# Kernel tuning notes

Measured on AMD Instinct MI355X. Metric: run time of the kernel, lower is better.

Reference implementation:

```python
import jax, jax.numpy as jnp
import numpy as np

B = 2
D = 256          # d_model == q_model
NH = 8           # heads
DH = D // NH
NP = 4           # sampling points per level
LV = 4           # feature levels
NQ = 4096        # queries
NL = 6           # encoder layers
DFF = 1024
SHAPES = [(128, 128), (64, 64), (32, 32), (16, 16)]
S = sum(h * w for h, w in SHAPES)


def setup_inputs() -> dict:
    key = jax.random.key(0)
    ks = iter(jax.random.split(key, 64))
    d = {}
    for l, (h, w) in enumerate(SHAPES):
        d[f"src{l}"] = jax.random.normal(next(ks), (B, D, h, w), jnp.float32)
        d[f"pos{l}"] = jax.random.normal(next(ks), (B, D, h, w), jnp.float32)
        d[f"mask{l}"] = jnp.zeros((B, h, w), jnp.bool_)
    d["q_feat"] = jax.random.normal(next(ks), (B, NQ, D), jnp.float32)
    d["q_pos"] = jax.random.normal(next(ks), (B, NQ, D), jnp.float32)
    d["q_ref"] = jax.random.uniform(next(ks), (B, NQ, 2), jnp.float32)
    d["level_embed"] = jax.random.normal(next(ks), (LV, D), jnp.float32) * 0.02

    def p(shape):
        return jax.random.normal(next(ks), shape, jnp.float32) * 0.02

    d["so_w"] = p((NL, NH * LV * NP * 2, D)); d["so_b"] = p((NL, NH * LV * NP * 2))
    d["aw_w"] = p((NL, NH * LV * NP, D));     d["aw_b"] = p((NL, NH * LV * NP))
    d["vp_w"] = p((NL, D, D)); d["vp_b"] = p((NL, D))
    d["op_w"] = p((NL, D, D)); d["op_b"] = p((NL, D))
    d["n1_g"] = jnp.ones((NL, D)); d["n1_b"] = jnp.zeros((NL, D))
    d["l1_w"] = p((NL, DFF, D)); d["l1_b"] = p((NL, DFF))
    d["l2_w"] = p((NL, D, DFF)); d["l2_b"] = p((NL, D))
    d["n2_g"] = jnp.ones((NL, D)); d["n2_b"] = jnp.zeros((NL, D))
    return d


def _ln(x, g, b):
    m = x.mean(-1, keepdims=True)
    v = ((x - m) ** 2).mean(-1, keepdims=True)
    return (x - m) * jax.lax.rsqrt(v + 1e-5) * g + b


def _bilinear(v, loc, Hl, Wl):
    # v: [B,NH,Hl*Wl,DH], loc: [B,NH,NQ,NP,2] normalized to [0,1]
    # grid_sample semantics, align_corners=False, zero padding
    x = loc[..., 0] * Wl - 0.5
    y = loc[..., 1] * Hl - 0.5
    x0 = jnp.floor(x); y0 = jnp.floor(y)
    wx = x - x0; wy = y - y0
    out = jnp.zeros((B, NH, NQ, NP, DH), v.dtype)
    for dx, dy in ((0, 0), (1, 0), (0, 1), (1, 1)):
        xc = x0 + dx; yc = y0 + dy
        w = (wx if dx else 1.0 - wx) * (wy if dy else 1.0 - wy)
        valid = (xc >= 0) & (xc < Wl) & (yc >= 0) & (yc < Hl)
        xi = jnp.clip(xc, 0, Wl - 1).astype(jnp.int32)
        yi = jnp.clip(yc, 0, Hl - 1).astype(jnp.int32)
        idx = (yi * Wl + xi).reshape(B, NH, NQ * NP)
        g = jnp.take_along_axis(v, idx[..., None], axis=2).reshape(B, NH, NQ, NP, DH)
        out = out + g * (w * valid)[..., None]
    return out


def _msda(q, ref, value, pad_mask, so_w, so_b, aw_w, aw_b, vp_w, vp_b, op_w, op_b):
    # q: [B,NQ,D]; ref: [B,NQ,LV,2]; value: [B,S,D]; pad_mask: [B,S] bool
    v = jnp.einsum('bsd,ed->bse', value, vp_w) + vp_b
    v = jnp.where(pad_mask[..., None], 0.0, v)
    v = v.reshape(B, S, NH, DH).transpose(0, 2, 1, 3)  # [B,NH,S,DH]
    offs = (jnp.einsum('bqd,od->bqo', q, so_w) + so_b).reshape(B, NQ, NH, LV, NP, 2)
    aw = (jnp.einsum('bqd,od->bqo', q, aw_w) + aw_b).reshape(B, NQ, NH, LV * NP)
    aw = jax.nn.softmax(aw, axis=-1).reshape(B, NQ, NH, LV, NP)
    norm = jnp.array([[w, h] for h, w in SHAPES], jnp.float32)  # (W,H) per level
    loc = ref[:, :, None, :, None, :] + offs / norm[None, None, None, :, None, :]
    loc = loc.transpose(0, 2, 1, 3, 4, 5)  # [B,NH,NQ,LV,NP,2]
    start = 0
    samp = []
    for l, (Hl, Wl) in enumerate(SHAPES):
        vl = v[:, :, start:start + Hl * Wl]
        start += Hl * Wl
        samp.append(_bilinear(vl, loc[:, :, :, l], Hl, Wl))
    samp = jnp.stack(samp, axis=3)  # [B,NH,NQ,LV,NP,DH]
    out = jnp.einsum('bhqlpd,bqhlp->bqhd', samp, aw).reshape(B, NQ, D)
    return jnp.einsum('bqd,od->bqo', out, op_w) + op_b


def _forward(srcs, poss, masks, q_feat, q_pos, q_ref, level_embed,
             so_w, so_b, aw_w, aw_b, vp_w, vp_b, op_w, op_b,
             n1_g, n1_b, l1_w, l1_b, l2_w, l2_b, n2_g, n2_b):
    src_flat, mask_flat = [], []
    for lvl, (s, m, p) in enumerate(zip(srcs, masks, poss)):
        b, c, h, w = s.shape
        src_flat.append(s.reshape(b, c, h * w).transpose(0, 2, 1))
        mask_flat.append(m.reshape(b, h * w))
        # lvl_pos_embed = p + level_embed[lvl]  (computed in torch but unused by layers)
    src_flat = jnp.concatenate(src_flat, axis=1)   # [B,S,D]
    mask_flat = jnp.concatenate(mask_flat, axis=1)  # [B,S]
    vrs = []
    for m in masks:
        _, H, W = m.shape
        vH = jnp.sum(~m[:, :, 0], axis=1).astype(jnp.float32) / H
        vW = jnp.sum(~m[:, 0, :], axis=1).astype(jnp.float32) / W
        vrs.append(jnp.stack([vW, vH], axis=-1))
    valid_ratios = jnp.stack(vrs, axis=1)  # [B,LV,2]
    ref = q_ref[:, :, None, :] * valid_ratios[:, None]  # [B,NQ,LV,2]
    qf = q_feat
    for l in range(NL):
        src2 = _msda(qf + q_pos, ref, src_flat, mask_flat,
                     so_w[l], so_b[l], aw_w[l], aw_b[l],
                     vp_w[l], vp_b[l], op_w[l], op_b[l])
        qf = _ln(qf + src2, n1_g[l], n1_b[l])
        h = jax.nn.relu(jnp.einsum('bqd,fd->bqf', qf, l1_w[l]) + l1_b[l])
        ff = jnp.einsum('bqf,df->bqd', h, l2_w[l]) + l2_b[l]
        qf = _ln(qf + ff, n2_g[l], n2_b[l])
    return qf


def reference(src0, src1, src2, src3, pos0, pos1, pos2, pos3,
              mask0, mask1, mask2, mask3, q_feat, q_pos, q_ref, level_embed,
              so_w, so_b, aw_w, aw_b, vp_w, vp_b, op_w, op_b,
              n1_g, n1_b, l1_w, l1_b, l2_w, l2_b, n2_g, n2_b):
    return _forward([src0, src1, src2, src3], [pos0, pos1, pos2, pos3],
                    [mask0, mask1, mask2, mask3], q_feat, q_pos, q_ref, level_embed,
                    so_w, so_b, aw_w, aw_b, vp_w, vp_b, op_w, op_b,
                    n1_g, n1_b, l1_w, l1_b, l2_w, l2_b, n2_g, n2_b)
```

## Files before the change

### kernel.cpp

```cpp
#include <hip/hip_runtime.h>
#include <math.h>

#define BB 2
#define DD 256
#define NH 8
#define DH 32
#define NPNP 4
#define LV 4
#define NQ 4096
#define NL 6
#define DFF 1024
#define SS 21760

typedef short v8s __attribute__((ext_vector_type(8)));
typedef float v4f __attribute__((ext_vector_type(4)));

__device__ __forceinline__ ushort f2b(float f) {
    union { float f; unsigned u; } v; v.f = f;
    unsigned r = v.u + 0x7fffu + ((v.u >> 16) & 1u);
    return (ushort)(r >> 16);
}

__device__ __constant__ int c_dims[4]   = {128, 64, 32, 16};
__device__ __constant__ int c_starts[4] = {0, 16384, 20480, 21504};
__device__ __constant__ int c_hw[4]     = {16384, 4096, 1024, 256};

__global__ __launch_bounds__(256) void flatten_all_kernel(
    const float* __restrict__ s0p, const float* __restrict__ s1p,
    const float* __restrict__ s2p, const float* __restrict__ s3p,
    ushort* __restrict__ dst)
{
    __shared__ float tile[64][65];
    int bx = blockIdx.x;
    int l, ls;
    if (bx < 256)      { l = 0; ls = bx; }
    else if (bx < 320) { l = 1; ls = bx - 256; }
    else if (bx < 336) { l = 2; ls = bx - 320; }
    else               { l = 3; ls = bx - 336; }
    const float* srcs[4] = {s0p, s1p, s2p, s3p};
    const float* src = srcs[l];
    const int HW = c_hw[l];
    const int start = c_starts[l];
    const int b  = blockIdx.z;
    const int d0 = blockIdx.y * 64;
    const int s0 = ls * 64;
    const int t  = threadIdx.x;
    const float* sp = src + ((size_t)b * DD + d0) * (size_t)HW + s0;
#pragma unroll
    for (int i = 0; i < 16; ++i) {
        int lin = i * 256 + t;
        int dl = lin >> 6, sl = lin & 63;
        tile[sl][dl] = sp[(size_t)dl * HW + sl];
    }
    __syncthreads();
    ushort* dp = dst + ((size_t)b * SS + start + s0) * DD + d0;
#pragma unroll
    for (int i = 0; i < 16; ++i) {
        int lin = i * 256 + t;
        int sl = lin >> 6, dl = lin & 63;
        dp[(size_t)sl * DD + dl] = f2b(tile[sl][dl]);
    }
}

__global__ __launch_bounds__(256) void cvt_all_kernel(
    const float* __restrict__ so, const float* __restrict__ aw,
    const float* __restrict__ vp, const float* __restrict__ op,
    const float* __restrict__ l1, const float* __restrict__ l2,
    ushort* __restrict__ qso, ushort* __restrict__ qaw,
    ushort* __restrict__ qvp, ushort* __restrict__ qop,
    ushort* __restrict__ ql1, ushort* __restrict__ ql2)
{
    int i = blockIdx.x * 256 + threadIdx.x;
    const float* in; ushort* out; int j;
    if (i < 98304)       { in = so; out = qso; j = i; }
    else if (i < 147456) { in = aw; out = qaw; j = i - 98304; }
    else if (i < 245760) { in = vp; out = qvp; j = i - 147456; }
    else if (i < 344064) { in = op; out = qop; j = i - 245760; }
    else if (i < 737280) { in = l1; out = ql1; j = i - 344064; }
    else                 { in = l2; out = ql2; j = i - 737280; }
    float4 x = ((const float4*)in)[j];
    uint2 pk;
    pk.x = (unsigned)f2b(x.x) | ((unsigned)f2b(x.y) << 16);
    pk.y = (unsigned)f2b(x.z) | ((unsigned)f2b(x.w) << 16);
    ((uint2*)out)[j] = pk;
}

__global__ __launch_bounds__(256) void add_bf_kernel(
    const float* __restrict__ a, const float* __restrict__ b,
    ushort* __restrict__ o, int n4)
{
    int i = blockIdx.x * 256 + threadIdx.x;
    if (i < n4) {
        float4 x = ((const float4*)a)[i];
        float4 y = ((const float4*)b)[i];
        uint2 pk;
        pk.x = (unsigned)f2b(x.x + y.x) | ((unsigned)f2b(x.y + y.y) << 16);
        pk.y = (unsigned)f2b(x.z + y.z) | ((unsigned)f2b(x.w + y.w) << 16);
        ((uint2*)o)[i] = pk;
    }
}

enum { EPI_PLAIN = 0, EPI_RELUB = 1, EPI_RES = 2, EPI_VSC = 3, EPI_QF = 4 };

template <int K, int EPI, int MF>
__global__ __launch_bounds__(256) void gemm_bf16(
    const ushort* __restrict__ A, const ushort* __restrict__ W,
    const float* __restrict__ bias, const float* __restrict__ res,
    void* __restrict__ out, int E,
    const ushort* __restrict__ W2, const float* __restrict__ bias2,
    void* __restrict__ out2)
{
    __shared__ ushort As[MF * 32 * 64];
    __shared__ ushort Ws[128 * 64];
    const int tid  = threadIdx.x;
    const int wave = tid >> 6, lane = tid & 63;
    const size_t r0 = (size_t)blockIdx.x * (MF * 32);
    const int e0 = blockIdx.y * 128;
    const int wrow = wave >> 1, wcol = wave & 1;

    const ushort* Wbase = W;
    const float*  bbase = bias;
    void* outp = out;
    int eoff = 0;
    if (EPI == EPI_VSC) {
        const size_t z = blockIdx.z;
        Wbase = W + z * (256 * 256);
        bbase = bias + z * 256;
        outp  = (void*)((ushort*)out + z * ((size_t)BB * NH * SS * DH));
    }
    if (EPI == EPI_QF && blockIdx.y == 2) {
        Wbase = W2; bbase = bias2; eoff = 256;
    }

    v4f acc[MF][4];
#pragma unroll
    for (int m = 0; m < MF; ++m)
#pragma unroll
        for (int n = 0; n < 4; ++n)
#pragma unroll
            for (int j = 0; j < 4; ++j) acc[m][n][j] = 0.f;

    const int srow   = lane >> 3;
    const int schunk = (lane & 7) ^ (srow & 7);
    const ushort* Ag = A + (r0 + wave * 8 + srow) * K + schunk * 8;
    const ushort* Wg = Wbase + ((size_t)(e0 - eoff + wave * 8 + srow)) * K + schunk * 8;

    for (int k0 = 0; k0 < K; k0 += 64) {
#pragma unroll
        for (int i = 0; i < MF; ++i) {
            __builtin_amdgcn_global_load_lds(
                (const __attribute__((address_space(1))) void*)(Ag + (size_t)(i * 32) * K + k0),
                (__attribute__((address_space(3))) void*)(As + (i * 32 + wave * 8) * 64),
                16, 0, 0);
        }
#pragma unroll
        for (int i = 0; i < 4; ++i) {
            __builtin_amdgcn_global_load_lds(
                (const __attribute__((address_space(1))) void*)(Wg + (size_t)(i * 32) * K + k0),
                (__attribute__((address_space(3))) void*)(Ws + (i * 32 + wave * 8) * 64),
                16, 0, 0);
        }
        __syncthreads();

        const int rlo = lane & 15;
#pragma unroll
        for (int ks = 0; ks < 2; ++ks) {
            const int chi = ks * 4 + (lane >> 4);
            v8s af[MF], bf[4];
#pragma unroll
            for (int m = 0; m < MF; ++m) {
                int r = wrow * (MF * 16) + m * 16 + rlo;
                af[m] = *(const v8s*)((const char*)As + r * 128 + ((chi ^ (r & 7)) << 4));
            }
#pragma unroll
            for (int n = 0; n < 4; ++n) {
                int r = wcol * 64 + n * 16 + rlo;
                bf[n] = *(const v8s*)((const char*)Ws + r * 128 + ((chi ^ (r & 7)) << 4));
            }
#pragma unroll
            for (int m = 0; m < MF; ++m)
#pragma unroll
                for (int n = 0; n < 4; ++n)
                    acc[m][n] = __builtin_amdgcn_mfma_f32_16x16x32_bf16(
                        af[m], bf[n], acc[m][n], 0, 0, 0);
        }
        __syncthreads();
    }

    const int lrow = (lane >> 4) << 2;
    const int lcol = lane & 15;
#pragma unroll
    for (int m = 0; m < MF; ++m) {
#pragma unroll
        for (int n = 0; n < 4; ++n) {
            const int ecol = e0 + wcol * 64 + n * 16 + lcol;
            const float bv = bbase[ecol - eoff];
#pragma unroll
            for (int j = 0; j < 4; ++j) {
                const size_t row = r0 + wrow * (MF * 16) + m * 16 + lrow + j;
                float val = acc[m][n][j] + bv;
                if (EPI == EPI_RELUB) {
                    ((ushort*)outp)[row * E + ecol] = f2b(fmaxf(val, 0.f));
                } else if (EPI == EPI_VSC) {
                    int b = (int)(row / SS), s = (int)(row % SS);
                    ((ushort*)outp)[(((size_t)b * NH + (ecol >> 5)) * SS + s) * DH + (ecol & 31)]
                        = f2b(val);
                } else if (EPI == EPI_RES) {
                    ((float*)outp)[row * E + ecol] = val + res[row * E + ecol];
                } else if (EPI == EPI_QF) {
                    if (eoff == 0) ((float*)outp)[row * 256 + ecol] = val;
                    else           ((float*)out2)[row * 128 + (ecol - 256)] = val;
                } else {
                    ((float*)outp)[row * E + ecol] = val;
                }
            }
        }
    }
}

__global__ __launch_bounds__(256) void msda_kernel(
    const ushort* __restrict__ v, const float* __restrict__ offs,
    const float* __restrict__ awb, const float* __restrict__ qref,
    ushort* __restrict__ out)
{
    __shared__ uint2 iw[4][128][4];
    const int wid  = threadIdx.x >> 6;
    const int lane = threadIdx.x & 63;
    const int gid  = blockIdx.x * 4 + wid;
    const int q = gid & (NQ - 1);
    const int b = gid >> 12;
    const size_t bq = (size_t)b * NQ + q;

    const float rx = qref[bq * 2 + 0];
    const float ry = qref[bq * 2 + 1];

#pragma unroll
    for (int it = 0; it < 2; ++it) {
        const int t = it * 64 + lane;
        const int pp = t & 15;
        const int lvl = pp >> 2;
        float a_raw = awb[bq * 128 + t];
        float mx = a_raw;
        mx = fmaxf(mx, __shfl_xor(mx, 1));
        mx = fmaxf(mx, __shfl_xor(mx, 2));
        mx = fmaxf(mx, __shfl_xor(mx, 4));
        mx = fmaxf(mx, __shfl_xor(mx, 8));
        float e = expf(a_raw - mx);
        float sum = e;
        sum += __shfl_xor(sum, 1);
        sum += __shfl_xor(sum, 2);
        sum += __shfl_xor(sum, 4);
        sum += __shfl_xor(sum, 8);
        const float a = e / sum;

        float2 oxy = *(const float2*)(offs + bq * 256 + t * 2);
        const int Wl = c_dims[lvl];
        const int st = c_starts[lvl];
        const float fW = (float)Wl;
        float x = fmaf(rx, fW, oxy.x) - 0.5f;
        float y = fmaf(ry, fW, oxy.y) - 0.5f;
        float x0f = floorf(x), y0f = floorf(y);
        float wx = x - x0f, wy = y - y0f;
        int x0 = (int)x0f, y0 = (int)y0f;
        const int hbase = (t >> 4) * SS;
#pragma unroll
        for (int c = 0; c < 4; ++c) {
            int dx = c & 1, dy = c >> 1;
            int xc = x0 + dx, yc = y0 + dy;
            bool valid = (xc >= 0) & (xc < Wl) & (yc >= 0) & (yc < Wl);
            int xi = min(max(xc, 0), Wl - 1);
            int yi = min(max(yc, 0), Wl - 1);
            float w = (dx ? wx : 1.f - wx) * (dy ? wy : 1.f - wy);
            uint2 tt;
            tt.x = (unsigned)((hbase + st + yi * Wl + xi) * (DH * 2));
            tt.y = __float_as_uint(valid ? a * w : 0.f);
            iw[wid][t][c] = tt;
        }
    }
    __syncthreads();

    const int c   = lane >> 4;
    const int dh2 = lane & 15;
    const char* vbase = (const char*)(v + (size_t)b * NH * SS * DH) + dh2 * 4;
#pragma unroll
    for (int h = 0; h < NH; ++h) {
        float acc0 = 0.f, acc1 = 0.f;
#pragma unroll
        for (int p = 0; p < 16; ++p) {
            uint2 t = iw[wid][h * 16 + p][c];
            float cw = __uint_as_float(t.y);
            unsigned v2 = *(const unsigned*)(vbase + t.x);
            float lo = __uint_as_float(v2 << 16);
            float hi = __uint_as_float(v2 & 0xffff0000u);
            acc0 = fmaf(cw, lo, acc0);
            acc1 = fmaf(cw, hi, acc1);
        }
        acc0 += __shfl_xor(acc0, 16); acc0 += __shfl_xor(acc0, 32);
        acc1 += __shfl_xor(acc1, 16); acc1 += __shfl_xor(acc1, 32);
        if (lane < 16) {
            unsigned pk = (unsigned)f2b(acc0) | ((unsigned)f2b(acc1) << 16);
            *(unsigned*)(out + bq * DD + h * DH + dh2 * 2) = pk;
        }
    }
}

__global__ __launch_bounds__(256) void ln_kernel(
    const float* __restrict__ x, const float* __restrict__ g,
    const float* __restrict__ bta, float* __restrict__ out,
    ushort* __restrict__ bfout, const float* __restrict__ pos)
{
    int row = blockIdx.x * 4 + (threadIdx.x >> 6);
    int lane = threadIdx.x & 63;
    const float* xp = x + (size_t)row * DD;
    float vals[4];
    float s = 0.f, s2 = 0.f;
#pragma unroll
    for (int j = 0; j < 4; ++j) {
        float vv = xp[j * 64 + lane];
        vals[j] = vv;
        s += vv; s2 += vv * vv;
    }
#pragma unroll
    for (int o = 32; o > 0; o >>= 1) {
        s  += __shfl_xor(s, o);
        s2 += __shfl_xor(s2, o);
    }
    float m = s * (1.f / DD);
    float var = s2 * (1.f / DD) - m * m;
    float r = rsqrtf(var + 1e-5f);
#pragma unroll
    for (int j = 0; j < 4; ++j) {
        int d = j * 64 + lane;
        float val = (vals[j] - m) * r * g[d] + bta[d];
        out[(size_t)row * DD + d] = val;
        if (bfout) {
            float bv = pos ? val + pos[(size_t)row * DD + d] : val;
            bfout[(size_t)row * DD + d] = f2b(bv);
        }
    }
}

extern "C" void kernel_launch(void* const* d_in, const int* in_sizes, int n_in,
                              void* d_out, int out_size, void* d_ws, size_t ws_size,
                              hipStream_t stream)
{
    const float* src[4]  = {(const float*)d_in[0], (const float*)d_in[3],
                            (const float*)d_in[6], (const float*)d_in[9]};
    const float* q_feat  = (const float*)d_in[12];
    const float* q_pos   = (const float*)d_in[13];
    const float* q_ref   = (const float*)d_in[14];
    const float* so_w = (const float*)d_in[16];
    const float* so_b = (const float*)d_in[17];
    const float* aw_w = (const float*)d_in[18];
    const float* aw_b = (const float*)d_in[19];
    const float* vp_w = (const float*)d_in[20];
    const float* vp_b = (const float*)d_in[21];
    const float* op_w = (const float*)d_in[22];
    const float* op_b = (const float*)d_in[23];
    const float* n1_g = (const float*)d_in[24];
    const float* n1_b = (const float*)d_in[25];
    const float* l1_w = (const float*)d_in[26];
    const float* l1_b = (const float*)d_in[27];
    const float* l2_w = (const float*)d_in[28];
    const float* l2_b = (const float*)d_in[29];
    const float* n2_g = (const float*)d_in[30];
    const float* n2_b = (const float*)d_in[31];

    char* p = (char*)d_ws;
    auto alloc = [&](size_t bytes) { char* r = p; p += (bytes + 255) & ~255ULL; return r; };

    ushort* src_flat = (ushort*)alloc((size_t)BB * SS * DD * 2);
    ushort* v_buf6   = (ushort*)alloc((size_t)NL * BB * NH * SS * DH * 2);
    ushort* q_bf     = (ushort*)alloc((size_t)BB * NQ * DD * 2);
    float*  offs     = (float*) alloc((size_t)BB * NQ * 256 * 4);
    float*  awb      = (float*) alloc((size_t)BB * NQ * 128 * 4);
    ushort* msda_bf  = (ushort*)alloc((size_t)BB * NQ * DD * 2);
    float*  tmp      = (float*) alloc((size_t)BB * NQ * DD * 4);
    ushort* hbuf     = (ushort*)alloc((size_t)BB * NQ * DFF * 2);
    ushort* qf_bf    = (ushort*)alloc((size_t)BB * NQ * DD * 2);
    ushort* w_so     = (ushort*)alloc((size_t)NL * 256 * 256 * 2);
    ushort* w_aw     = (ushort*)alloc((size_t)NL * 128 * 256 * 2);
    ushort* w_vp     = (ushort*)alloc((size_t)NL * 256 * 256 * 2);
    ushort* w_op     = (ushort*)alloc((size_t)NL * 256 * 256 * 2);
    ushort* w_l1     = (ushort*)alloc((size_t)NL * DFF * 256 * 2);
    ushort* w_l2     = (ushort*)alloc((size_t)NL * 256 * DFF * 2);

    float* qf = (float*)d_out;

    cvt_all_kernel<<<4416, 256, 0, stream>>>(
        so_w, aw_w, vp_w, op_w, l1_w, l2_w,
        w_so, w_aw, w_vp, w_op, w_l1, w_l2);

    flatten_all_kernel<<<dim3(340, 4, 2), 256, 0, stream>>>(
        src[0], src[1], src[2], src[3], src_flat);

    const int RQ = BB * NQ;
    const int RV = BB * SS;

    add_bf_kernel<<<RQ * DD / (256 * 4), 256, 0, stream>>>(q_feat, q_pos, q_bf, RQ * DD / 4);

    gemm_bf16<256, EPI_VSC, 4><<<dim3(RV / 128, 2, NL), 256, 0, stream>>>(
        src_flat, w_vp, vp_b, nullptr, v_buf6, 256, nullptr, nullptr, nullptr);

    for (int l = 0; l < NL; ++l) {
        const float* so_bl = so_b + (size_t)l * 256;
        const float* aw_bl = aw_b + (size_t)l * 128;
        const float* op_bl = op_b + (size_t)l * 256;
        const float* l1_bl = l1_b + (size_t)l * DFF;
        const float* l2_bl = l2_b + (size_t)l * 256;

        gemm_bf16<256, EPI_QF, 2><<<dim3(RQ / 64, 3), 256, 0, stream>>>(
            q_bf, w_so + (size_t)l * 256 * 256, so_bl, nullptr, offs, 256,
            w_aw + (size_t)l * 128 * 256, aw_bl, awb);

        msda_kernel<<<(BB * NQ) / 4, 256, 0, stream>>>(
            v_buf6 + (size_t)l * BB * NH * SS * DH, offs, awb, q_ref, msda_bf);

        gemm_bf16<256, EPI_RES, 2><<<dim3(RQ / 64, 2), 256, 0, stream>>>(
            msda_bf, w_op + (size_t)l * 256 * 256, op_bl,
            (l == 0 ? q_feat : qf), tmp, 256, nullptr, nullptr, nullptr);
        ln_kernel<<<RQ / 4, 256, 0, stream>>>(tmp, n1_g + l * 256, n1_b + l * 256,
                                              qf, qf_bf, nullptr);

        gemm_bf16<256, EPI_RELUB, 4><<<dim3(RQ / 128, DFF / 128), 256, 0, stream>>>(
            qf_bf, w_l1 + (size_t)l * DFF * 256, l1_bl, nullptr, hbuf, DFF,
            nullptr, nullptr, nullptr);
        gemm_bf16<1024, EPI_RES, 2><<<dim3(RQ / 64, 2), 256, 0, stream>>>(
            hbuf, w_l2 + (size_t)l * 256 * DFF, l2_bl, qf, tmp, 256,
            nullptr, nullptr, nullptr);
        ln_kernel<<<RQ / 4, 256, 0, stream>>>(tmp, n2_g + l * 256, n2_b + l * 256,
                                              qf, q_bf, q_pos);
    }

    (void)in_sizes; (void)n_in; (void)out_size; (void)ws_size;
}
```

Measured before the change: 598.6 us.

## Fuse residual GEMMs with LayerNorm and reuse A tile across value projections

Replaces the output-projection and FFN2 GEMMs plus separate LayerNorm kernels with a single gemm_ln_kernel that computes a full 256-wide row block, adds bias and residual, and performs LayerNorm in the epilogue. This removes the fp32 temp buffer round trip and two launches per layer. The value projection now loads the A tile once into LDS and loops over all six layers' weights, avoiding rereading src_flat six times. In exchange, the fused GEMM uses 32-row blocks (256 blocks), which lowers parallelism, and it reads and writes qf in place.

```diff
diff --git a/kernel.cpp b/kernel.cpp
--- a/kernel.cpp
+++ b/kernel.cpp
@@ -100,13 +100,106 @@
     }
 }
 
-enum { EPI_PLAIN = 0, EPI_RELUB = 1, EPI_RES = 2, EPI_VSC = 3, EPI_QF = 4 };
+__global__ __launch_bounds__(256) void vp_gemm_kernel(
+    const ushort* __restrict__ A, const ushort* __restrict__ W,
+    const float* __restrict__ bias, ushort* __restrict__ out)
+{
+    __shared__ ushort As[64 * 256];
+    __shared__ ushort Ws[128 * 64];
+    const int tid  = threadIdx.x;
+    const int wave = tid >> 6, lane = tid & 63;
+    const size_t r0 = (size_t)blockIdx.x * 64;
+    const int e0 = blockIdx.y * 128;
+    const int wrow = wave >> 1, wcol = wave & 1;
+
+#pragma unroll
+    for (int i = 0; i < 8; ++i) {
+        int lin = i * 256 + tid;
+        int row = lin >> 5;
+        int cs  = lin & 31;
+        int sc  = cs ^ (row & 7);
+        __builtin_amdgcn_global_load_lds(
+            (const __attribute__((address_space(1))) void*)(A + (r0 + row) * 256 + sc * 8),
+            (__attribute__((address_space(3))) void*)(As + (size_t)lin * 8),
+            16, 0, 0);
+    }
+
+    const int srow   = lane >> 3;
+    const int schunk = (lane & 7) ^ (srow & 7);
+    const int rlo  = lane & 15;
+    const int lrow = (lane >> 4) << 2;
+    const int lcol = lane & 15;
+
+    for (int z = 0; z < NL; ++z) {
+        const ushort* Wz = W + (size_t)z * 256 * 256;
+        v4f acc[2][4];
+#pragma unroll
+        for (int m = 0; m < 2; ++m)
+#pragma unroll
+            for (int n = 0; n < 4; ++n)
+#pragma unroll
+                for (int j = 0; j < 4; ++j) acc[m][n][j] = 0.f;
+
+        for (int k0 = 0; k0 < 256; k0 += 64) {
+#pragma unroll
+            for (int i = 0; i < 4; ++i) {
+                __builtin_amdgcn_global_load_lds(
+                    (const __attribute__((address_space(1))) void*)(
+                        Wz + (size_t)(e0 + i * 32 + wave * 8 + srow) * 256 + k0 + schunk * 8),
+                    (__attribute__((address_space(3))) void*)(Ws + (i * 32 + wave * 8) * 64),
+                    16, 0, 0);
+            }
+            __syncthreads();
+#pragma unroll
+            for (int ks = 0; ks < 2; ++ks) {
+                const int chiA = (k0 >> 3) + ks * 4 + (lane >> 4);
+                const int chiW = ks * 4 + (lane >> 4);
+                v8s af[2], bf[4];
+#pragma unroll
+                for (int m = 0; m < 2; ++m) {
+                    int r = wrow * 32 + m * 16 + rlo;
+                    af[m] = *(const v8s*)((const char*)As + r * 512 + ((chiA ^ (r & 7)) << 4));
+                }
+#pragma unroll
+                for (int n = 0; n < 4; ++n) {
+                    int r = wcol * 64 + n * 16 + rlo;
+                    bf[n] = *(const v8s*)((const char*)Ws + r * 128 + ((chiW ^ (r & 7)) << 4));
+                }
+#pragma unroll
+                for (int m = 0; m < 2; ++m)
+#pragma unroll
+                    for (int n = 0; n < 4; ++n)
+                        acc[m][n] = __builtin_amdgcn_mfma_f32_16x16x32_bf16(
+                            af[m], bf[n], acc[m][n], 0, 0, 0);
+            }
+            __syncthreads();
+        }
+
+        ushort* outz = out + (size_t)z * BB * NH * SS * DH;
+#pragma unroll
+        for (int m = 0; m < 2; ++m) {
+#pragma unroll
+            for (int n = 0; n < 4; ++n) {
+                const int ecol = e0 + wcol * 64 + n * 16 + lcol;
+                const float bv = bias[z * 256 + ecol];
+#pragma unroll
+                for (int j = 0; j < 4; ++j) {
+                    const size_t row = r0 + wrow * 32 + m * 16 + lrow + j;
+                    int b = (int)(row / SS), s = (int)(row % SS);
+                    outz[(((size_t)b * NH + (ecol >> 5)) * SS + s) * DH + (ecol & 31)]
+                        = f2b(acc[m][n][j] + bv);
+                }
+            }
+        }
+    }
+}
+
+enum { EPI_RELUB = 1, EPI_QF = 4 };
 
 template <int K, int EPI, int MF>
 __global__ __launch_bounds__(256) void gemm_bf16(
     const ushort* __restrict__ A, const ushort* __restrict__ W,
-    const float* __restrict__ bias, const float* __restrict__ res,
-    void* __restrict__ out, int E,
+    const float* __restrict__ bias, void* __restrict__ out, int E,
     const ushort* __restrict__ W2, const float* __restrict__ bias2,
     void* __restrict__ out2)
 {
@@ -120,14 +213,7 @@
 
     const ushort* Wbase = W;
     const float*  bbase = bias;
-    void* outp = out;
     int eoff = 0;
-    if (EPI == EPI_VSC) {
-        const size_t z = blockIdx.z;
-        Wbase = W + z * (256 * 256);
-        bbase = bias + z * 256;
-        outp  = (void*)((ushort*)out + z * ((size_t)BB * NH * SS * DH));
-    }
     if (EPI == EPI_QF && blockIdx.y == 2) {
         Wbase = W2; bbase = bias2; eoff = 256;
     }
@@ -200,20 +286,126 @@
                 const size_t row = r0 + wrow * (MF * 16) + m * 16 + lrow + j;
                 float val = acc[m][n][j] + bv;
                 if (EPI == EPI_RELUB) {
-                    ((ushort*)outp)[row * E + ecol] = f2b(fmaxf(val, 0.f));
-                } else if (EPI == EPI_VSC) {
-                    int b = (int)(row / SS), s = (int)(row % SS);
-                    ((ushort*)outp)[(((size_t)b * NH + (ecol >> 5)) * SS + s) * DH + (ecol & 31)]
-                        = f2b(val);
-                } else if (EPI == EPI_RES) {
-                    ((float*)outp)[row * E + ecol] = val + res[row * E + ecol];
-                } else if (EPI == EPI_QF) {
-                    if (eoff == 0) ((float*)outp)[row * 256 + ecol] = val;
+                    ((ushort*)out)[row * E + ecol] = f2b(fmaxf(val, 0.f));
+                } else {
+                    if (eoff == 0) ((float*)out)[row * 256 + ecol] = val;
                     else           ((float*)out2)[row * 128 + (ecol - 256)] = val;
-                } else {
-                    ((float*)outp)[row * E + ecol] = val;
                 }
             }
+        }
+    }
+}
+
+template <int K, bool ADDPOS>
+__global__ __launch_bounds__(256) void gemm_ln_kernel(
+    const ushort* __restrict__ A, const ushort* __restrict__ W,
+    const float* __restrict__ bias, const float* __restrict__ res,
+    const float* __restrict__ g, const float* __restrict__ beta,
+    float* __restrict__ outF, ushort* __restrict__ outB,
+    const float* __restrict__ pos)
+{
+    __shared__ ushort As[32 * 64];
+    __shared__ ushort Ws[256 * 64];
+    __shared__ float rsum[2][32], rsq[2][32];
+    const int tid  = threadIdx.x;
+    const int wave = tid >> 6, lane = tid & 63;
+    const size_t r0 = (size_t)blockIdx.x * 32;
+    const int wrow = wave >> 1, wcol = wave & 1;
+    const int rlo = lane & 15;
+
+    v4f acc[8];
+#pragma unroll
+    for (int n = 0; n < 8; ++n)
+#pragma unroll
+        for (int j = 0; j < 4; ++j) acc[n][j] = 0.f;
+
+    const int arow = tid >> 3;
+    const int asc  = (tid & 7) ^ (arow & 7);
+
+    for (int k0 = 0; k0 < K; k0 += 64) {
+        __builtin_amdgcn_global_load_lds(
+            (const __attribute__((address_space(1))) void*)(A + (r0 + arow) * K + k0 + asc * 8),
+            (__attribute__((address_space(3))) void*)(As + (size_t)tid * 8),
+            16, 0, 0);
+#pragma unroll
+        for (int i = 0; i < 8; ++i) {
+            int lin = i * 256 + tid;
+            int wr = lin >> 3;
+            int wsc = (lin & 7) ^ (wr & 7);
+            __builtin_amdgcn_global_load_lds(
+                (const __attribute__((address_space(1))) void*)(W + (size_t)wr * K + k0 + wsc * 8),
+                (__attribute__((address_space(3))) void*)(Ws + (size_t)lin * 8),
+                16, 0, 0);
+        }
+        __syncthreads();
+#pragma unroll
+        for (int ks = 0; ks < 2; ++ks) {
+            const int chi = ks * 4 + (lane >> 4);
+            const int ra = wrow * 16 + rlo;
+            v8s af = *(const v8s*)((const char*)As + ra * 128 + ((chi ^ (ra & 7)) << 4));
+            v8s bf[8];
+#pragma unroll
+            for (int n = 0; n < 8; ++n) {
+                int rb = wcol * 128 + n * 16 + rlo;
+                bf[n] = *(const v8s*)((const char*)Ws + rb * 128 + ((chi ^ (rb & 7)) << 4));
+            }
+#pragma unroll
+            for (int n = 0; n < 8; ++n)
+                acc[n] = __builtin_amdgcn_mfma_f32_16x16x32_bf16(af, bf[n], acc[n], 0, 0, 0);
+        }
+        __syncthreads();
+    }
+
+    const int lrow = (lane >> 4) << 2;
+    const int lcol = lane & 15;
+    float sums[4] = {0.f, 0.f, 0.f, 0.f};
+    float sqs[4]  = {0.f, 0.f, 0.f, 0.f};
+#pragma unroll
+    for (int n = 0; n < 8; ++n) {
+        const int ecol = wcol * 128 + n * 16 + lcol;
+        const float bv = bias[ecol];
+#pragma unroll
+        for (int j = 0; j < 4; ++j) {
+            const size_t row = r0 + wrow * 16 + lrow + j;
+            float v = acc[n][j] + bv + res[row * 256 + ecol];
+            acc[n][j] = v;
+            sums[j] += v;
+            sqs[j]  += v * v;
+        }
+    }
+#pragma unroll
+    for (int off = 1; off < 16; off <<= 1) {
+#pragma unroll
+        for (int j = 0; j < 4; ++j) {
+            sums[j] += __shfl_xor(sums[j], off);
+            sqs[j]  += __shfl_xor(sqs[j], off);
+        }
+    }
+    if ((lane & 15) == 0) {
+#pragma unroll
+        for (int j = 0; j < 4; ++j) {
+            int ridx = wrow * 16 + lrow + j;
+            rsum[wcol][ridx] = sums[j];
+            rsq[wcol][ridx]  = sqs[j];
+        }
+    }
+    __syncthreads();
+#pragma unroll
+    for (int j = 0; j < 4; ++j) {
+        const int ridx = wrow * 16 + lrow + j;
+        const float s  = rsum[0][ridx] + rsum[1][ridx];
+        const float sq = rsq[0][ridx] + rsq[1][ridx];
+        const float mean = s * (1.f / 256.f);
+        const float var  = sq * (1.f / 256.f) - mean * mean;
+        const float rstd = rsqrtf(var + 1e-5f);
+        const size_t row = r0 + wrow * 16 + lrow + j;
+#pragma unroll
+        for (int n = 0; n < 8; ++n) {
+            const int ecol = wcol * 128 + n * 16 + lcol;
+            float o = (acc[n][j] - mean) * rstd * g[ecol] + beta[ecol];
+            outF[row * 256 + ecol] = o;
+            float ob = ADDPOS ? (o + pos[row * 256 + ecol]) : o;
+            outB[row * 256 + ecol] = f2b(ob);
         }
     }
 }
@@ -300,42 +492,6 @@
         if (lane < 16) {
             unsigned pk = (unsigned)f2b(acc0) | ((unsigned)f2b(acc1) << 16);
             *(unsigned*)(out + bq * DD + h * DH + dh2 * 2) = pk;
-        }
-    }
-}
-
-__global__ __launch_bounds__(256) void ln_kernel(
-    const float* __restrict__ x, const float* __restrict__ g,
-    const float* __restrict__ bta, float* __restrict__ out,
-    ushort* __restrict__ bfout, const float* __restrict__ pos)
-{
-    int row = blockIdx.x * 4 + (threadIdx.x >> 6);
-    int lane = threadIdx.x & 63;
-    const float* xp = x + (size_t)row * DD;
-    float vals[4];
-    float s = 0.f, s2 = 0.f;
-#pragma unroll
-    for (int j = 0; j < 4; ++j) {
-        float vv = xp[j * 64 + lane];
-        vals[j] = vv;
-        s += vv; s2 += vv * vv;
-    }
-#pragma unroll
-    for (int o = 32; o > 0; o >>= 1) {
-        s  += __shfl_xor(s, o);
-        s2 += __shfl_xor(s2, o);
-    }
-    float m = s * (1.f / DD);
-    float var = s2 * (1.f / DD) - m * m;
-    float r = rsqrtf(var + 1e-5f);
-#pragma unroll
-    for (int j = 0; j < 4; ++j) {
-        int d = j * 64 + lane;
-        float val = (vals[j] - m) * r * g[d] + bta[d];
-        out[(size_t)row * DD + d] = val;
-        if (bfout) {
-            float bv = pos ? val + pos[(size_t)row * DD + d] : val;
-            bfout[(size_t)row * DD + d] = f2b(bv);
         }
     }
 }
@@ -375,7 +531,6 @@
     float*  offs     = (float*) alloc((size_t)BB * NQ * 256 * 4);
     float*  awb      = (float*) alloc((size_t)BB * NQ * 128 * 4);
     ushort* msda_bf  = (ushort*)alloc((size_t)BB * NQ * DD * 2);
-    float*  tmp      = (float*) alloc((size_t)BB * NQ * DD * 4);
     ushort* hbuf     = (ushort*)alloc((size_t)BB * NQ * DFF * 2);
     ushort* qf_bf    = (ushort*)alloc((size_t)BB * NQ * DD * 2);
     ushort* w_so     = (ushort*)alloc((size_t)NL * 256 * 256 * 2);
@@ -399,37 +554,30 @@
 
     add_bf_kernel<<<RQ * DD / (256 * 4), 256, 0, stream>>>(q_feat, q_pos, q_bf, RQ * DD / 4);
 
-    gemm_bf16<256, EPI_VSC, 4><<<dim3(RV / 128, 2, NL), 256, 0, stream>>>(
-        src_flat, w_vp, vp_b, nullptr, v_buf6, 256, nullptr, nullptr, nullptr);
+    vp_gemm_kernel<<<dim3(RV / 64, 2), 256, 0, stream>>>(
+        src_flat, w_vp, vp_b, v_buf6);
 
     for (int l = 0; l < NL; ++l) {
-        const float* so_bl = so_b + (size_t)l * 256;
-        const float* aw_bl = aw_b + (size_t)l * 128;
-        const float* op_bl = op_b + (size_t)l * 256;
-        const float* l1_bl = l1_b + (size_t)l * DFF;
-        const float* l2_bl = l2_b + (size_t)l * 256;
-
         gemm_bf16<256, EPI_QF, 2><<<dim3(RQ / 64, 3), 256, 0, stream>>>(
-            q_bf, w_so + (size_t)l * 256 * 256, so_bl, nullptr, offs, 256,
-            w_aw + (size_t)l * 128 * 256, aw_bl, awb);
+            q_bf, w_so + (size_t)l * 256 * 256, so_b + (size_t)l * 256, offs, 256,
+            w_aw + (size_t)l * 128 * 256, aw_b + (size_t)l * 128, awb);
 
         msda_kernel<<<(BB * NQ) / 4, 256, 0, stream>>>(
             v_buf6 + (size_t)l * BB * NH * SS * DH, offs, awb, q_ref, msda_bf);
 
-        gemm_bf16<256, EPI_RES, 2><<<dim3(RQ / 64, 2), 256, 0, stream>>>(
-            msda_bf, w_op + (size_t)l * 256 * 256, op_bl,
-            (l == 0 ? q_feat : qf), tmp, 256, nullptr, nullptr, nullptr);
-        ln_kernel<<<RQ / 4, 256, 0, stream>>>(tmp, n1_g + l * 256, n1_b + l * 256,
-                                              qf, qf_bf, nullptr);
+        gemm_ln_kernel<256, false><<<RQ / 32, 256, 0, stream>>>(
+            msda_bf, w_op + (size_t)l * 256 * 256, op_b + (size_t)l * 256,
+            (l == 0 ? q_feat : qf), n1_g + l * 256, n1_b + l * 256,
+            qf, qf_bf, nullptr);
 
         gemm_bf16<256, EPI_RELUB, 4><<<dim3(RQ / 128, DFF / 128), 256, 0, stream>>>(
-            qf_bf, w_l1 + (size_t)l * DFF * 256, l1_bl, nullptr, hbuf, DFF,
+            qf_bf, w_l1 + (size_t)l * DFF * 256, l1_b + (size_t)l * DFF, hbuf, DFF,
             nullptr, nullptr, nullptr);
-        gemm_bf16<1024, EPI_RES, 2><<<dim3(RQ / 64, 2), 256, 0, stream>>>(
-            hbuf, w_l2 + (size_t)l * 256 * DFF, l2_bl, qf, tmp, 256,
-            nullptr, nullptr, nullptr);
-        ln_kernel<<<RQ / 4, 256, 0, stream>>>(tmp, n2_g + l * 256, n2_b + l * 256,
-                                              qf, q_bf, q_pos);
+
+        gemm_ln_kernel<1024, true><<<RQ / 32, 256, 0, stream>>>(
+            hbuf, w_l2 + (size_t)l * 256 * DFF, l2_b + (size_t)l * 256,
+            qf, n2_g + l * 256, n2_b + l * 256,
+            qf, q_bf, q_pos);
     }
 
     (void)in_sizes; (void)n_in; (void)out_size; (void)ws_size;
```

Result: faster. 554.1 us (-7.4%).
